# Performance work log

Measured on AMD Instinct MI355X. Metric: run time of the kernel, lower is better.

The kernel has to match this reference:

```python
import jax, jax.numpy as jnp
import numpy as np

D = 768       # input_dim / model width
H = 3072      # expert hidden width (init arg 'output_dim')
E = 8         # num_experts
K = 2         # top_k
NOISE_STD = 0.1
B, S = 2, 1024


def setup_inputs() -> dict:
    key = jax.random.key(0)
    ks = jax.random.split(key, 16)
    sd = lambda fan_in: 1.0 / np.sqrt(fan_in)
    return {
        "x": jax.random.normal(ks[0], (B, S, D), dtype=jnp.float32),
        "noise": jax.random.normal(ks[1], (B, S, E), dtype=jnp.float32),
        # router
        "Wr": jax.random.normal(ks[2], (D, E), dtype=jnp.float32) * sd(D),
        "br": jnp.zeros((E,), dtype=jnp.float32),
        # stacked expert FFNs: d -> h -> d
        "W1": jax.random.normal(ks[3], (E, D, H), dtype=jnp.float32) * sd(D),
        "b1": jnp.zeros((E, H), dtype=jnp.float32),
        "W2": jax.random.normal(ks[4], (E, H, D), dtype=jnp.float32) * sd(H),
        "b2": jnp.zeros((E, D), dtype=jnp.float32),
        # shared expert
        "Ws1": jax.random.normal(ks[5], (D, H), dtype=jnp.float32) * sd(D),
        "bs1": jnp.zeros((H,), dtype=jnp.float32),
        "Ws2": jax.random.normal(ks[6], (H, D), dtype=jnp.float32) * sd(H),
        "bs2": jnp.zeros((D,), dtype=jnp.float32),
        # mixing scalars (alpha trainable, beta frozen in torch)
        "alpha": jnp.float32(0.3),
        "beta": jnp.float32(0.7),
    }


def reference(x, noise, Wr, br, W1, b1, W2, b2, Ws1, bs1, Ws2, bs2, alpha, beta):
    b, s, d = x.shape
    xt = x.reshape(-1, d)                       # [T, D]
    nt = noise.reshape(-1, E)                   # [T, E]
    T = xt.shape[0]

    # router: noisy logits -> top-k -> softmax over selected experts only
    logits = xt @ Wr + br + NOISE_STD * nt      # [T, E]
    top_vals, top_idx = jax.lax.top_k(logits, K)  # [T, K]
    top_w = jax.nn.softmax(top_vals, axis=-1)     # softmax over -inf-masked logits == softmax over top-k
    gates = jnp.zeros((T, E), dtype=x.dtype).at[jnp.arange(T)[:, None], top_idx].set(top_w)  # [T, E], 0 elsewhere

    # experts (dense over E; non-selected contributions are zeroed by gates)
    h = jax.nn.leaky_relu(jnp.einsum('td,edh->teh', xt, W1) + b1, negative_slope=0.01)  # [T, E, H]
    y = jnp.einsum('teh,ehd->ted', h, W2) + b2                                          # [T, E, D]
    moe_out = jnp.einsum('ted,te->td', y, gates)                                        # [T, D]

    # shared expert
    sh = jax.nn.leaky_relu(xt @ Ws1 + bs1, negative_slope=0.01)
    shared_out = sh @ Ws2 + bs2                                                         # [T, D]

    w = jax.nn.softmax(jnp.stack([alpha, beta]))
    out = shared_out * w[0] + moe_out * w[1]
    return out.reshape(b, s, d)
```

## Files before the change

### kernel.cpp

```cpp
#include <hip/hip_runtime.h>
#include <hip/hip_bf16.h>
#include <cstdio>
#include <cstdint>

#define TNUM 2048
#define DDIM 768
#define HDIM 3072
#define ENUM 8

#define WAITVM(N) asm volatile("s_waitcnt vmcnt(" #N ")" ::: "memory")
#define MEMFENCE() asm volatile("" ::: "memory")

typedef __attribute__((ext_vector_type(8))) __bf16 bf16x8;
typedef __attribute__((ext_vector_type(4))) float f32x4;

__device__ __forceinline__ unsigned short f2bf(float f) {
    __bf16 h = (__bf16)f;
    unsigned short u;
    __builtin_memcpy(&u, &h, 2);
    return u;
}

__device__ __forceinline__ void async_cp16(const unsigned short* g, unsigned short* l) {
    __builtin_amdgcn_global_load_lds((const __attribute__((address_space(1))) void*)g,
                                     (__attribute__((address_space(3))) void*)l,
                                     16, 0, 0);
}

__device__ __forceinline__ void transpose_tile(const float* __restrict__ in,
                                               unsigned short* __restrict__ out,
                                               int R, int C, int c0, int r0,
                                               unsigned int* tileT32) {
    int tid = threadIdx.x;
    int l15 = tid & 15;
    int g = tid >> 4;
    int par = (g >> 1) & 1;
    int hf = g & 1;
    int cb = hf * 64 + l15 * 4;
    #pragma unroll
    for (int p = 0; p < 16; p++) {
        int unit = p * 16 + g;
        int r = unit >> 1;
        float4 v = *(const float4*)(in + (size_t)(r0 + r) * C + c0 + cb);
        unsigned int m01 = (unsigned int)f2bf(v.x) | ((unsigned int)f2bf(v.y) << 16);
        unsigned int m23 = (unsigned int)f2bf(v.z) | ((unsigned int)f2bf(v.w) << 16);
        unsigned int o01 = __shfl_xor(m01, 32);
        unsigned int o23 = __shfl_xor(m23, 32);
        unsigned int wA = par ? ((o23 & 0xffffu) | (m23 << 16))
                              : ((m01 & 0xffffu) | (o01 << 16));
        unsigned int wB = par ? ((o23 >> 16) | (m23 & 0xffff0000u))
                              : ((m01 >> 16) | (o01 & 0xffff0000u));
        int ca = cb + par * 2;
        int rp = unit >> 2;
        int cq = ca >> 2;
        int woff = 4 * (((rp >> 2) + 3 * cq) & 15) + (((rp & 3) + cq) & 3);
        tileT32[ca * 68 + woff] = wA;
        tileT32[(ca + 1) * 68 + woff] = wB;
    }
    __syncthreads();
    #pragma unroll
    for (int p = 0; p < 8; p++) {
        int cc = p * 16 + g;
        int cqp = cc >> 2;
        const uint4 W = *(const uint4*)&tileT32[cc * 68 + 4 * ((l15 + 3 * cqp) & 15)];
        unsigned int a0 = W.x, a1 = W.y, a2 = W.z, a3 = W.w;
        int rsel = cqp & 3;
        if (rsel & 1) { unsigned int t = a0; a0 = a1; a1 = a2; a2 = a3; a3 = t; }
        if (rsel & 2) { unsigned int t0 = a0, t1 = a1; a0 = a2; a1 = a3; a2 = t0; a3 = t1; }
        uint4 ov; ov.x = a0; ov.y = a1; ov.z = a2; ov.w = a3;
        *(uint4*)(out + (size_t)(c0 + cc) * R + r0 + l15 * 8) = ov;
    }
}

__global__ __launch_bounds__(256)
void pre_kernel(const float* __restrict__ x, const float* __restrict__ noise,
                const float* __restrict__ Wr, const float* __restrict__ br,
                const float* __restrict__ W1, const float* __restrict__ Ws1,
                unsigned short* __restrict__ W1t, unsigned short* __restrict__ Ws1t,
                unsigned short* __restrict__ xb,
                int* __restrict__ counts, int* __restrict__ list,
                int* __restrict__ inv, float* __restrict__ tokp) {
    __shared__ __align__(16) unsigned int tileT32[128 * 68];
    int b = blockIdx.x;
    if (b < 1296) {
        int m = b / 144, t = b % 144;
        const float* in       = (m < 8) ? (W1 + (size_t)m * DDIM * HDIM) : Ws1;
        unsigned short* out   = (m < 8) ? (W1t + (size_t)m * HDIM * DDIM) : Ws1t;
        transpose_tile(in, out, DDIM, HDIM, (t % 24) * 128, (t / 24) * 128, tileT32);
        return;
    }
    if (b < 2064) {
        int i = ((b - 1296) * 256 + threadIdx.x) * 8;
        float4 a = *(const float4*)(x + i);
        float4 bb = *(const float4*)(x + i + 4);
        ushort4 lo = make_ushort4(f2bf(a.x), f2bf(a.y), f2bf(a.z), f2bf(a.w));
        ushort4 hi = make_ushort4(f2bf(bb.x), f2bf(bb.y), f2bf(bb.z), f2bf(bb.w));
        *(ushort4*)(xb + i) = lo;
        *(ushort4*)(xb + i + 4) = hi;
        return;
    }
    int lane = threadIdx.x & 63;
    int t = (b - 2064) * 4 + (threadIdx.x >> 6);
    float acc[8];
    #pragma unroll
    for (int e = 0; e < 8; e++) acc[e] = 0.f;
    #pragma unroll
    for (int i = 0; i < 12; i++) {
        int d = i * 64 + lane;
        float xv = x[t * DDIM + d];
        float4 w0 = *(const float4*)(Wr + d * 8);
        float4 w1 = *(const float4*)(Wr + d * 8 + 4);
        acc[0] += xv * w0.x; acc[1] += xv * w0.y; acc[2] += xv * w0.z; acc[3] += xv * w0.w;
        acc[4] += xv * w1.x; acc[5] += xv * w1.y; acc[6] += xv * w1.z; acc[7] += xv * w1.w;
    }
    #pragma unroll
    for (int e = 0; e < 8; e++) {
        #pragma unroll
        for (int off2 = 32; off2 >= 1; off2 >>= 1)
            acc[e] += __shfl_xor(acc[e], off2, 64);
    }
    if (lane == 0) {
        float lg[8];
        #pragma unroll
        for (int e = 0; e < 8; e++) lg[e] = acc[e] + br[e] + 0.1f * noise[t * 8 + e];
        int e0 = 0;
        #pragma unroll
        for (int e = 1; e < 8; e++) if (lg[e] > lg[e0]) e0 = e;
        int e1 = -1;
        #pragma unroll
        for (int e = 0; e < 8; e++) if (e != e0 && (e1 < 0 || lg[e] > lg[e1])) e1 = e;
        float m = fmaxf(lg[e0], lg[e1]);
        float p0 = expf(lg[e0] - m), p1 = expf(lg[e1] - m);
        float inv_s = 1.f / (p0 + p1);
        int s0 = atomicAdd(&counts[e0], 1);
        list[e0 * TNUM + s0] = t;
        int s1 = atomicAdd(&counts[e1], 1);
        list[e1 * TNUM + s1] = t;
        inv[t * 2 + 0] = (e0 << 16) | s0;
        inv[t * 2 + 1] = (e1 << 16) | s1;
        tokp[t * 2 + 0] = p0 * inv_s;
        tokp[t * 2 + 1] = p1 * inv_s;
    }
}

__global__ __launch_bounds__(256, 3)
void ffn1_kernel(const unsigned short* __restrict__ xb,
                 const unsigned short* __restrict__ W1t,
                 const unsigned short* __restrict__ Ws1t,
                 const float* __restrict__ b1, const float* __restrict__ bs1,
                 const int* __restrict__ counts, const int* __restrict__ list,
                 unsigned short* __restrict__ hbuf,
                 const float* __restrict__ W2, const float* __restrict__ Ws2,
                 unsigned short* __restrict__ W2t, unsigned short* __restrict__ Ws2t) {
    __shared__ __align__(16) unsigned char smem[49152];

    if (blockIdx.z >= 3) {
        int q = (blockIdx.z - 3) * 384 + blockIdx.y * 8 + blockIdx.x;
        if (q >= 1296) return;
        int m = q / 144, t = q % 144;
        const float* in     = (m < 8) ? (W2 + (size_t)m * HDIM * DDIM) : Ws2;
        unsigned short* out = (m < 8) ? (W2t + (size_t)m * DDIM * HDIM) : Ws2t;
        transpose_tile(in, out, HDIM, DDIM, (t % 6) * 128, (t / 6) * 128, (unsigned int*)smem);
        return;
    }

    unsigned short* As = (unsigned short*)smem;
    unsigned short* Bs = (unsigned short*)(smem + 24576);

    int j = blockIdx.z * 8 + blockIdx.x;
    int y = blockIdx.y;
    int mt0 = y / 12, ntl = y % 12;

    int offv[8];
    { int s = 0;
      #pragma unroll
      for (int e = 0; e < 8; e++) { offv[e] = s; s += counts[e]; } }

    int cnt, hbase, n0, mbase, ntiles;
    const unsigned short* Bmat;
    const float* bias;
    const int* lst = nullptr;
    if (j < 16) {
        int e = j >> 1, nh = j & 1;
        cnt = counts[e];
        ntiles = (cnt + 127) >> 7;
        mbase = 0;
        hbase = offv[e];
        n0 = nh * 1536 + ntl * 128;
        Bmat = W1t + (size_t)e * HDIM * DDIM;
        bias = b1 + e * HDIM;
        lst = list + e * TNUM;
    } else {
        int q = j - 16;
        int ms = q >> 1, nh = q & 1;
        mbase = ms * 512;
        ntiles = 4;
        cnt = 1 << 30;
        hbase = 2 * TNUM;
        n0 = nh * 1536 + ntl * 128;
        Bmat = Ws1t;
        bias = bs1;
    }
    if (mt0 >= ntiles) return;

    int tid = threadIdx.x;
    int w = tid >> 6, lane = tid & 63;
    int l15 = lane & 15, quad = lane >> 4;
    int wm = (w & 1) * 64, wn = (w >> 1) * 64;
    int rcA = (w & 1) * 4;
    int rcB = (w >> 1) * 4;
    const int KT = DDIM / 32;

    const unsigned short* gB[2];
    int ldsoff[2], rowl[2];
    #pragma unroll
    for (int r = 0; r < 2; r++) {
        int rc = r * 4 + w;
        rowl[r] = rc * 16 + l15;
        ldsoff[r] = rc * 512;
        gB[r] = Bmat + (size_t)(n0 + rowl[r]) * DDIM + quad * 8;
    }

    for (int mt = mt0; mt < ntiles; mt += 4) {
        int m0 = mbase + mt * 128;
        const unsigned short* gA[2];
        #pragma unroll
        for (int r = 0; r < 2; r++) {
            int row;
            if (lst) row = lst[min(m0 + rowl[r], cnt - 1)];
            else     row = m0 + rowl[r];
            gA[r] = xb + (size_t)row * DDIM + quad * 8;
        }

        f32x4 zero = {0.f, 0.f, 0.f, 0.f};
        f32x4 acc[4][4];
        #pragma unroll
        for (int i = 0; i < 4; i++)
            #pragma unroll
            for (int jj = 0; jj < 4; jj++) acc[i][jj] = zero;

        __builtin_amdgcn_s_barrier();
        MEMFENCE();
        #pragma unroll
        for (int t = 0; t < 2; t++)
            #pragma unroll
            for (int r = 0; r < 2; r++) {
                async_cp16(gA[r] + t * 32, As + t * 4096 + ldsoff[r]);
                async_cp16(gB[r] + t * 32, Bs + t * 4096 + ldsoff[r]);
            }

        #pragma unroll 1
        for (int kt = 0; kt < KT; kt++) {
            if (kt == KT - 1) { WAITVM(0); } else { WAITVM(4); }
            __builtin_amdgcn_s_barrier();
            MEMFENCE();
            int cur = kt % 3;
            if (kt + 2 < KT) {
                int nb = (kt + 2) % 3;
                int ko = (kt + 2) * 32;
                #pragma unroll
                for (int r = 0; r < 2; r++) {
                    async_cp16(gA[r] + ko, As + nb * 4096 + ldsoff[r]);
                    async_cp16(gB[r] + ko, Bs + nb * 4096 + ldsoff[r]);
                }
            }
            bf16x8 af[4], bv[4];
            #pragma unroll
            for (int i = 0; i < 4; i++)
                af[i] = *(const bf16x8*)(As + cur * 4096 + ((rcA + i) * 64 + quad * 16 + l15) * 8);
            #pragma unroll
            for (int jj = 0; jj < 4; jj++)
                bv[jj] = *(const bf16x8*)(Bs + cur * 4096 + ((rcB + jj) * 64 + quad * 16 + l15) * 8);
            #pragma unroll
            for (int i = 0; i < 4; i++)
                #pragma unroll
                for (int jj = 0; jj < 4; jj++)
                    acc[i][jj] = __builtin_amdgcn_mfma_f32_16x16x32_bf16(af[i], bv[jj], acc[i][jj], 0, 0, 0);
        }

        #pragma unroll
        for (int i = 0; i < 4; i++) {
            int rbase = m0 + wm + i * 16 + quad * 4;
            #pragma unroll
            for (int jj = 0; jj < 4; jj++) {
                int gc = n0 + wn + jj * 16 + l15;
                float bvl = bias[gc];
                #pragma unroll
                for (int r = 0; r < 4; r++) {
                    int gr = rbase + r;
                    if (gr < cnt) {
                        float v = acc[i][jj][r] + bvl;
                        v = v > 0.f ? v : 0.01f * v;
                        hbuf[(size_t)(hbase + gr) * HDIM + gc] = f2bf(v);
                    }
                }
            }
        }
    }
}

__global__ __launch_bounds__(256, 4)
void ffn2_kernel(const unsigned short* __restrict__ hbuf,
                 const unsigned short* __restrict__ W2t,
                 const unsigned short* __restrict__ Ws2t,
                 const int* __restrict__ counts,
                 float* __restrict__ ybuf) {
    __shared__ __align__(16) unsigned short As[3][256 * 8];
    __shared__ __align__(16) unsigned short Bs[3][512 * 8];

    int j = blockIdx.z * 8 + blockIdx.x;
    int y = blockIdx.y;
    int mt0 = y / 6, ntl = y % 6;
    int n0 = ntl * 128;

    int offv[8];
    { int s = 0;
      #pragma unroll
      for (int e = 0; e < 8; e++) { offv[e] = s; s += counts[e]; } }

    int cnt, hbase, mbase, ntiles;
    const unsigned short* Bmat;
    if (j < 8) {
        int e = j;
        cnt = counts[e];
        ntiles = (cnt + 63) >> 6;
        mbase = 0;
        hbase = offv[e];
        Bmat = W2t + (size_t)e * DDIM * HDIM;
    } else {
        int s = j - 8;
        mbase = s * 256;
        ntiles = 4;
        cnt = 1 << 30;
        hbase = 2 * TNUM;
        Bmat = Ws2t;
    }
    if (mt0 >= ntiles) return;

    int tid = threadIdx.x;
    int w = tid >> 6, lane = tid & 63;
    int l15 = lane & 15, quad = lane >> 4;
    int wm = (w & 1) * 32, wn = (w >> 1) * 64;
    int rcA = (w & 1) * 2;
    int rcB = (w >> 1) * 4;
    const int KT = HDIM / 32;
    int rowl = w * 16 + l15;

    const unsigned short* gB[2];
    int ldsoffB[2];
    #pragma unroll
    for (int r = 0; r < 2; r++) {
        int rc = r * 4 + w;
        gB[r] = Bmat + (size_t)(n0 + rc * 16 + l15) * HDIM + quad * 8;
        ldsoffB[r] = rc * 512;
    }

    for (int mt = mt0; mt < ntiles; mt += 8) {
        int m0 = mbase + mt * 64;
        int ra = (j < 8) ? min(m0 + rowl, cnt - 1) : (m0 + rowl);
        const unsigned short* gA0 = hbuf + (size_t)(hbase + ra) * HDIM + quad * 8;

        f32x4 zero = {0.f, 0.f, 0.f, 0.f};
        f32x4 acc[2][4];
        #pragma unroll
        for (int i = 0; i < 2; i++)
            #pragma unroll
            for (int jj = 0; jj < 4; jj++) acc[i][jj] = zero;

        __builtin_amdgcn_s_barrier();
        MEMFENCE();
        #pragma unroll
        for (int t = 0; t < 2; t++) {
            async_cp16(gA0 + t * 32, &As[t][w * 512]);
            #pragma unroll
            for (int r = 0; r < 2; r++) async_cp16(gB[r] + t * 32, &Bs[t][ldsoffB[r]]);
        }

        #pragma unroll 1
        for (int kt = 0; kt < KT; kt++) {
            if (kt == KT - 1) { WAITVM(0); } else { WAITVM(3); }
            __builtin_amdgcn_s_barrier();
            MEMFENCE();
            int cur = kt % 3;
            if (kt + 2 < KT) {
                int nb = (kt + 2) % 3;
                int ko = (kt + 2) * 32;
                async_cp16(gA0 + ko, &As[nb][w * 512]);
                #pragma unroll
                for (int r = 0; r < 2; r++) async_cp16(gB[r] + ko, &Bs[nb][ldsoffB[r]]);
            }
            bf16x8 af[2], bv[4];
            #pragma unroll
            for (int i = 0; i < 2; i++)
                af[i] = *(const bf16x8*)&As[cur][((rcA + i) * 64 + quad * 16 + l15) * 8];
            #pragma unroll
            for (int jj = 0; jj < 4; jj++)
                bv[jj] = *(const bf16x8*)&Bs[cur][((rcB + jj) * 64 + quad * 16 + l15) * 8];
            #pragma unroll
            for (int i = 0; i < 2; i++)
                #pragma unroll
                for (int jj = 0; jj < 4; jj++)
                    acc[i][jj] = __builtin_amdgcn_mfma_f32_16x16x32_bf16(af[i], bv[jj], acc[i][jj], 0, 0, 0);
        }

        #pragma unroll
        for (int i = 0; i < 2; i++) {
            int rbase = m0 + wm + i * 16 + quad * 4;
            #pragma unroll
            for (int r = 0; r < 4; r++) {
                int gr = rbase + r;
                if (gr >= cnt) continue;
                float* orow = ybuf + (size_t)(hbase + gr) * DDIM + n0 + wn;
                #pragma unroll
                for (int jj = 0; jj < 4; jj++)
                    orow[jj * 16 + l15] = acc[i][jj][r];
            }
        }
    }
}

__global__ void mix_kernel(const float* __restrict__ ybuf, const int* __restrict__ inv,
                           const float* __restrict__ tokp, const int* __restrict__ counts,
                           const float* __restrict__ b2, const float* __restrict__ bs2,
                           const float* __restrict__ alpha, const float* __restrict__ beta,
                           float* __restrict__ out) {
    int t = blockIdx.x;
    int c = threadIdx.x * 4;
    int offv[8];
    { int s = 0;
      #pragma unroll
      for (int e = 0; e < 8; e++) { offv[e] = s; s += counts[e]; } }
    float a = alpha[0], bsc = beta[0];
    float m = fmaxf(a, bsc);
    float ea = expf(a - m), eb = expf(bsc - m);
    float is = 1.f / (ea + eb);
    float ws = ea * is, wmx = eb * is;

    int i0 = inv[t * 2 + 0], i1 = inv[t * 2 + 1];
    int e0 = i0 >> 16, sl0 = i0 & 0xFFFF;
    int e1 = i1 >> 16, sl1 = i1 & 0xFFFF;
    float p0 = tokp[t * 2 + 0], p1 = tokp[t * 2 + 1];
    size_t rA = (size_t)(offv[e0] + sl0) * DDIM + c;
    size_t rB = (size_t)(offv[e1] + sl1) * DDIM + c;
    size_t rS = (size_t)(2 * TNUM + t) * DDIM + c;
    float4 vA = *(const float4*)(ybuf + rA);
    float4 vB = *(const float4*)(ybuf + rB);
    float4 vS = *(const float4*)(ybuf + rS);
    float4 bA = *(const float4*)(b2 + e0 * DDIM + c);
    float4 bB = *(const float4*)(b2 + e1 * DDIM + c);
    float4 bS = *(const float4*)(bs2 + c);
    float4 o;
    o.x = ws * (vS.x + bS.x) + wmx * (p0 * (vA.x + bA.x) + p1 * (vB.x + bB.x));
    o.y = ws * (vS.y + bS.y) + wmx * (p0 * (vA.y + bA.y) + p1 * (vB.y + bB.y));
    o.z = ws * (vS.z + bS.z) + wmx * (p0 * (vA.z + bA.z) + p1 * (vB.z + bB.z));
    o.w = ws * (vS.w + bS.w) + wmx * (p0 * (vA.w + bA.w) + p1 * (vB.w + bB.w));
    *(float4*)(out + (size_t)t * DDIM + c) = o;
}

extern "C" void kernel_launch(void* const* d_in, const int* in_sizes, int n_in,
                              void* d_out, int out_size, void* d_ws, size_t ws_size,
                              hipStream_t stream) {
    const float* x     = (const float*)d_in[0];
    const float* noise = (const float*)d_in[1];
    const float* Wr    = (const float*)d_in[2];
    const float* br    = (const float*)d_in[3];
    const float* W1    = (const float*)d_in[4];
    const float* b1    = (const float*)d_in[5];
    const float* W2    = (const float*)d_in[6];
    const float* b2    = (const float*)d_in[7];
    const float* Ws1   = (const float*)d_in[8];
    const float* bs1   = (const float*)d_in[9];
    const float* Ws2   = (const float*)d_in[10];
    const float* bs2   = (const float*)d_in[11];
    const float* alpha = (const float*)d_in[12];
    const float* beta  = (const float*)d_in[13];

    char* ws = (char*)d_ws;
    size_t off = 0;
    auto alloc = [&](size_t bytes) -> char* {
        char* p = ws + off;
        off = (off + bytes + 255) & ~(size_t)255;
        return p;
    };
    int*   counts = (int*)  alloc(ENUM * 4);
    int*   list   = (int*)  alloc((size_t)ENUM * TNUM * 4);
    int*   inv    = (int*)  alloc((size_t)TNUM * 2 * 4);
    float* tokp   = (float*)alloc((size_t)TNUM * 2 * 4);
    unsigned short* xb   = (unsigned short*)alloc((size_t)TNUM * DDIM * 2);
    unsigned short* W1t  = (unsigned short*)alloc((size_t)ENUM * HDIM * DDIM * 2);
    unsigned short* Ws1t = (unsigned short*)alloc((size_t)HDIM * DDIM * 2);
    unsigned short* W2t  = (unsigned short*)alloc((size_t)ENUM * DDIM * HDIM * 2);
    unsigned short* Ws2t = (unsigned short*)alloc((size_t)DDIM * HDIM * 2);
    unsigned short* hbuf = (unsigned short*)alloc((size_t)(3 * TNUM) * HDIM * 2);
    float* ybuf = (float*)W1t;
    if (off > ws_size) {
        fprintf(stderr, "kernel_launch: workspace too small (need %zu, have %zu)\n", off, ws_size);
        return;
    }

    hipMemsetAsync(counts, 0, ENUM * 4, stream);

    pre_kernel<<<dim3(2576), dim3(256), 0, stream>>>(x, noise, Wr, br, W1, Ws1,
                                                     W1t, Ws1t, xb, counts, list, inv, tokp);
    ffn1_kernel<<<dim3(8, 48, 7), dim3(256), 0, stream>>>(xb, W1t, Ws1t, b1, bs1, counts, list,
                                                          hbuf, W2, Ws2, W2t, Ws2t);
    ffn2_kernel<<<dim3(8, 48, 2), dim3(256), 0, stream>>>(hbuf, W2t, Ws2t, counts, ybuf);
    mix_kernel<<<dim3(TNUM), dim3(192), 0, stream>>>(ybuf, inv, tokp, counts, b2, bs2,
                                                     alpha, beta, (float*)d_out);
}
```

Baseline: 506.7 us.

## Split-K the second FFN, double-buffer GEMM loops, move W2 transposes to pre-kernel

```diff
diff --git a/kernel.cpp b/kernel.cpp
--- a/kernel.cpp
+++ b/kernel.cpp
@@ -76,7 +76,9 @@
 void pre_kernel(const float* __restrict__ x, const float* __restrict__ noise,
                 const float* __restrict__ Wr, const float* __restrict__ br,
                 const float* __restrict__ W1, const float* __restrict__ Ws1,
+                const float* __restrict__ W2, const float* __restrict__ Ws2,
                 unsigned short* __restrict__ W1t, unsigned short* __restrict__ Ws1t,
+                unsigned short* __restrict__ W2t, unsigned short* __restrict__ Ws2t,
                 unsigned short* __restrict__ xb,
                 int* __restrict__ counts, int* __restrict__ list,
                 int* __restrict__ inv, float* __restrict__ tokp) {
@@ -89,8 +91,16 @@
         transpose_tile(in, out, DDIM, HDIM, (t % 24) * 128, (t / 24) * 128, tileT32);
         return;
     }
-    if (b < 2064) {
-        int i = ((b - 1296) * 256 + threadIdx.x) * 8;
+    if (b < 2592) {
+        int q = b - 1296;
+        int m = q / 144, t = q % 144;
+        const float* in     = (m < 8) ? (W2 + (size_t)m * HDIM * DDIM) : Ws2;
+        unsigned short* out = (m < 8) ? (W2t + (size_t)m * DDIM * HDIM) : Ws2t;
+        transpose_tile(in, out, HDIM, DDIM, (t % 6) * 128, (t / 6) * 128, tileT32);
+        return;
+    }
+    if (b < 3360) {
+        int i = ((b - 2592) * 256 + threadIdx.x) * 8;
         float4 a = *(const float4*)(x + i);
         float4 bb = *(const float4*)(x + i + 4);
         ushort4 lo = make_ushort4(f2bf(a.x), f2bf(a.y), f2bf(a.z), f2bf(a.w));
@@ -100,7 +110,7 @@
         return;
     }
     int lane = threadIdx.x & 63;
-    int t = (b - 2064) * 4 + (threadIdx.x >> 6);
+    int t = (b - 3360) * 4 + (threadIdx.x >> 6);
     float acc[8];
     #pragma unroll
     for (int e = 0; e < 8; e++) acc[e] = 0.f;
@@ -143,29 +153,16 @@
     }
 }
 
-__global__ __launch_bounds__(256, 3)
+
+__global__ __launch_bounds__(256, 4)
 void ffn1_kernel(const unsigned short* __restrict__ xb,
                  const unsigned short* __restrict__ W1t,
                  const unsigned short* __restrict__ Ws1t,
                  const float* __restrict__ b1, const float* __restrict__ bs1,
                  const int* __restrict__ counts, const int* __restrict__ list,
-                 unsigned short* __restrict__ hbuf,
-                 const float* __restrict__ W2, const float* __restrict__ Ws2,
-                 unsigned short* __restrict__ W2t, unsigned short* __restrict__ Ws2t) {
-    __shared__ __align__(16) unsigned char smem[49152];
-
-    if (blockIdx.z >= 3) {
-        int q = (blockIdx.z - 3) * 384 + blockIdx.y * 8 + blockIdx.x;
-        if (q >= 1296) return;
-        int m = q / 144, t = q % 144;
-        const float* in     = (m < 8) ? (W2 + (size_t)m * HDIM * DDIM) : Ws2;
-        unsigned short* out = (m < 8) ? (W2t + (size_t)m * DDIM * HDIM) : Ws2t;
-        transpose_tile(in, out, HDIM, DDIM, (t % 6) * 128, (t / 6) * 128, (unsigned int*)smem);
-        return;
-    }
-
-    unsigned short* As = (unsigned short*)smem;
-    unsigned short* Bs = (unsigned short*)(smem + 24576);
+                 unsigned short* __restrict__ hbuf) {
+    __shared__ __align__(16) unsigned short As[2][512 * 8];
+    __shared__ __align__(16) unsigned short Bs[2][512 * 8];
 
     int j = blockIdx.z * 8 + blockIdx.x;
     int y = blockIdx.y;
@@ -239,14 +236,12 @@
             #pragma unroll
             for (int jj = 0; jj < 4; jj++) acc[i][jj] = zero;
 
-        __builtin_amdgcn_s_barrier();
-        MEMFENCE();
         #pragma unroll
         for (int t = 0; t < 2; t++)
             #pragma unroll
             for (int r = 0; r < 2; r++) {
-                async_cp16(gA[r] + t * 32, As + t * 4096 + ldsoff[r]);
-                async_cp16(gB[r] + t * 32, Bs + t * 4096 + ldsoff[r]);
+                async_cp16(gA[r] + t * 32, &As[t][ldsoff[r]]);
+                async_cp16(gB[r] + t * 32, &Bs[t][ldsoff[r]]);
             }
 
         #pragma unroll 1
@@ -254,28 +249,30 @@
             if (kt == KT - 1) { WAITVM(0); } else { WAITVM(4); }
             __builtin_amdgcn_s_barrier();
             MEMFENCE();
-            int cur = kt % 3;
-            if (kt + 2 < KT) {
-                int nb = (kt + 2) % 3;
-                int ko = (kt + 2) * 32;
-                #pragma unroll
-                for (int r = 0; r < 2; r++) {
-                    async_cp16(gA[r] + ko, As + nb * 4096 + ldsoff[r]);
-                    async_cp16(gB[r] + ko, Bs + nb * 4096 + ldsoff[r]);
-                }
-            }
+            int cur = kt & 1;
             bf16x8 af[4], bv[4];
             #pragma unroll
             for (int i = 0; i < 4; i++)
-                af[i] = *(const bf16x8*)(As + cur * 4096 + ((rcA + i) * 64 + quad * 16 + l15) * 8);
+                af[i] = *(const bf16x8*)&As[cur][((rcA + i) * 64 + quad * 16 + l15) * 8];
             #pragma unroll
             for (int jj = 0; jj < 4; jj++)
-                bv[jj] = *(const bf16x8*)(Bs + cur * 4096 + ((rcB + jj) * 64 + quad * 16 + l15) * 8);
+                bv[jj] = *(const bf16x8*)&Bs[cur][((rcB + jj) * 64 + quad * 16 + l15) * 8];
             #pragma unroll
             for (int i = 0; i < 4; i++)
                 #pragma unroll
                 for (int jj = 0; jj < 4; jj++)
                     acc[i][jj] = __builtin_amdgcn_mfma_f32_16x16x32_bf16(af[i], bv[jj], acc[i][jj], 0, 0, 0);
+            MEMFENCE();
+            __builtin_amdgcn_s_barrier();
+            MEMFENCE();
+            if (kt + 2 < KT) {
+                int ko = (kt + 2) * 32;
+                #pragma unroll
+                for (int r = 0; r < 2; r++) {
+                    async_cp16(gA[r] + ko, &As[cur][ldsoff[r]]);
+                    async_cp16(gB[r] + ko, &Bs[cur][ldsoff[r]]);
+                }
+            }
         }
 
         #pragma unroll
@@ -305,8 +302,8 @@
                  const unsigned short* __restrict__ Ws2t,
                  const int* __restrict__ counts,
                  float* __restrict__ ybuf) {
-    __shared__ __align__(16) unsigned short As[3][256 * 8];
-    __shared__ __align__(16) unsigned short Bs[3][512 * 8];
+    __shared__ __align__(16) unsigned short As[2][256 * 8];
+    __shared__ __align__(16) unsigned short Bs[2][512 * 8];
 
     int j = blockIdx.z * 8 + blockIdx.x;
     int y = blockIdx.y;
@@ -318,24 +315,26 @@
       #pragma unroll
       for (int e = 0; e < 8; e++) { offv[e] = s; s += counts[e]; } }
 
-    int cnt, hbase, mbase, ntiles;
+    int cnt, hbase, mbase, kh, ntiles;
     const unsigned short* Bmat;
-    if (j < 8) {
-        int e = j;
+    if (j < 16) {
+        int e = j >> 1; kh = j & 1;
         cnt = counts[e];
         ntiles = (cnt + 63) >> 6;
         mbase = 0;
         hbase = offv[e];
         Bmat = W2t + (size_t)e * DDIM * HDIM;
     } else {
-        int s = j - 8;
-        mbase = s * 256;
-        ntiles = 4;
+        int q = j - 16;
+        int mh = q >> 1; kh = q & 1;
+        mbase = mh * 512;
+        ntiles = 8;
         cnt = 1 << 30;
         hbase = 2 * TNUM;
         Bmat = Ws2t;
     }
     if (mt0 >= ntiles) return;
+    int kbase = kh * (HDIM / 2);
 
     int tid = threadIdx.x;
     int w = tid >> 6, lane = tid & 63;
@@ -343,7 +342,7 @@
     int wm = (w & 1) * 32, wn = (w >> 1) * 64;
     int rcA = (w & 1) * 2;
     int rcB = (w >> 1) * 4;
-    const int KT = HDIM / 32;
+    const int KT = (HDIM / 2) / 32;
     int rowl = w * 16 + l15;
 
     const unsigned short* gB[2];
@@ -351,14 +350,15 @@
     #pragma unroll
     for (int r = 0; r < 2; r++) {
         int rc = r * 4 + w;
-        gB[r] = Bmat + (size_t)(n0 + rc * 16 + l15) * HDIM + quad * 8;
+        gB[r] = Bmat + (size_t)(n0 + rc * 16 + l15) * HDIM + kbase + quad * 8;
         ldsoffB[r] = rc * 512;
     }
+    float* yb = ybuf + (size_t)kh * 6144 * DDIM;
 
     for (int mt = mt0; mt < ntiles; mt += 8) {
         int m0 = mbase + mt * 64;
-        int ra = (j < 8) ? min(m0 + rowl, cnt - 1) : (m0 + rowl);
-        const unsigned short* gA0 = hbuf + (size_t)(hbase + ra) * HDIM + quad * 8;
+        int ra = (j < 16) ? min(m0 + rowl, cnt - 1) : (m0 + rowl);
+        const unsigned short* gA0 = hbuf + (size_t)(hbase + ra) * HDIM + kbase + quad * 8;
 
         f32x4 zero = {0.f, 0.f, 0.f, 0.f};
         f32x4 acc[2][4];
@@ -367,8 +367,6 @@
             #pragma unroll
             for (int jj = 0; jj < 4; jj++) acc[i][jj] = zero;
 
-        __builtin_amdgcn_s_barrier();
-        MEMFENCE();
         #pragma unroll
         for (int t = 0; t < 2; t++) {
             async_cp16(gA0 + t * 32, &As[t][w * 512]);
@@ -381,14 +379,7 @@
             if (kt == KT - 1) { WAITVM(0); } else { WAITVM(3); }
             __builtin_amdgcn_s_barrier();
             MEMFENCE();
-            int cur = kt % 3;
-            if (kt + 2 < KT) {
-                int nb = (kt + 2) % 3;
-                int ko = (kt + 2) * 32;
-                async_cp16(gA0 + ko, &As[nb][w * 512]);
-                #pragma unroll
-                for (int r = 0; r < 2; r++) async_cp16(gB[r] + ko, &Bs[nb][ldsoffB[r]]);
-            }
+            int cur = kt & 1;
             bf16x8 af[2], bv[4];
             #pragma unroll
             for (int i = 0; i < 2; i++)
@@ -401,6 +392,15 @@
                 #pragma unroll
                 for (int jj = 0; jj < 4; jj++)
                     acc[i][jj] = __builtin_amdgcn_mfma_f32_16x16x32_bf16(af[i], bv[jj], acc[i][jj], 0, 0, 0);
+            MEMFENCE();
+            __builtin_amdgcn_s_barrier();
+            MEMFENCE();
+            if (kt + 2 < KT) {
+                int ko = (kt + 2) * 32;
+                async_cp16(gA0 + ko, &As[cur][w * 512]);
+                #pragma unroll
+                for (int r = 0; r < 2; r++) async_cp16(gB[r] + ko, &Bs[cur][ldsoffB[r]]);
+            }
         }
 
         #pragma unroll
@@ -410,7 +410,7 @@
             for (int r = 0; r < 4; r++) {
                 int gr = rbase + r;
                 if (gr >= cnt) continue;
-                float* orow = ybuf + (size_t)(hbase + gr) * DDIM + n0 + wn;
+                float* orow = yb + (size_t)(hbase + gr) * DDIM + n0 + wn;
                 #pragma unroll
                 for (int jj = 0; jj < 4; jj++)
                     orow[jj * 16 + l15] = acc[i][jj][r];
@@ -443,17 +443,22 @@
     size_t rA = (size_t)(offv[e0] + sl0) * DDIM + c;
     size_t rB = (size_t)(offv[e1] + sl1) * DDIM + c;
     size_t rS = (size_t)(2 * TNUM + t) * DDIM + c;
-    float4 vA = *(const float4*)(ybuf + rA);
-    float4 vB = *(const float4*)(ybuf + rB);
-    float4 vS = *(const float4*)(ybuf + rS);
+    const float* y0 = ybuf;
+    const float* y1 = ybuf + (size_t)6144 * DDIM;
+    float4 vA0 = *(const float4*)(y0 + rA);
+    float4 vA1 = *(const float4*)(y1 + rA);
+    float4 vB0 = *(const float4*)(y0 + rB);
+    float4 vB1 = *(const float4*)(y1 + rB);
+    float4 vS0 = *(const float4*)(y0 + rS);
+    float4 vS1 = *(const float4*)(y1 + rS);
     float4 bA = *(const float4*)(b2 + e0 * DDIM + c);
     float4 bB = *(const float4*)(b2 + e1 * DDIM + c);
     float4 bS = *(const float4*)(bs2 + c);
     float4 o;
-    o.x = ws * (vS.x + bS.x) + wmx * (p0 * (vA.x + bA.x) + p1 * (vB.x + bB.x));
-    o.y = ws * (vS.y + bS.y) + wmx * (p0 * (vA.y + bA.y) + p1 * (vB.y + bB.y));
-    o.z = ws * (vS.z + bS.z) + wmx * (p0 * (vA.z + bA.z) + p1 * (vB.z + bB.z));
-    o.w = ws * (vS.w + bS.w) + wmx * (p0 * (vA.w + bA.w) + p1 * (vB.w + bB.w));
+    o.x = ws * (vS0.x + vS1.x + bS.x) + wmx * (p0 * (vA0.x + vA1.x + bA.x) + p1 * (vB0.x + vB1.x + bB.x));
+    o.y = ws * (vS0.y + vS1.y + bS.y) + wmx * (p0 * (vA0.y + vA1.y + bA.y) + p1 * (vB0.y + vB1.y + bB.y));
+    o.z = ws * (vS0.z + vS1.z + bS.z) + wmx * (p0 * (vA0.z + vA1.z + bA.z) + p1 * (vB0.z + vB1.z + bB.z));
+    o.w = ws * (vS0.w + vS1.w + bS.w) + wmx * (p0 * (vA0.w + vA1.w + bA.w) + p1 * (vB0.w + vB1.w + bB.w));
     *(float4*)(out + (size_t)t * DDIM + c) = o;
 }
 
@@ -500,11 +505,11 @@
 
     hipMemsetAsync(counts, 0, ENUM * 4, stream);
 
-    pre_kernel<<<dim3(2576), dim3(256), 0, stream>>>(x, noise, Wr, br, W1, Ws1,
-                                                     W1t, Ws1t, xb, counts, list, inv, tokp);
-    ffn1_kernel<<<dim3(8, 48, 7), dim3(256), 0, stream>>>(xb, W1t, Ws1t, b1, bs1, counts, list,
-                                                          hbuf, W2, Ws2, W2t, Ws2t);
-    ffn2_kernel<<<dim3(8, 48, 2), dim3(256), 0, stream>>>(hbuf, W2t, Ws2t, counts, ybuf);
+    pre_kernel<<<dim3(3872), dim3(256), 0, stream>>>(x, noise, Wr, br, W1, Ws1, W2, Ws2,
+                                                     W1t, Ws1t, W2t, Ws2t, xb,
+                                                     counts, list, inv, tokp);
+    ffn1_kernel<<<dim3(8, 48, 3), dim3(256), 0, stream>>>(xb, W1t, Ws1t, b1, bs1, counts, list, hbuf);
+    ffn2_kernel<<<dim3(8, 48, 3), dim3(256), 0, stream>>>(hbuf, W2t, Ws2t, counts, ybuf);
     mix_kernel<<<dim3(TNUM), dim3(192), 0, stream>>>(ybuf, inv, tokp, counts, b2, bs2,
                                                      alpha, beta, (float*)d_out);
 }
```

After: 443.6 us. -12.4%, faster.
